# Optimization experiments

Measured on AMD Instinct MI355X. Metric: run time of the kernel, lower is better.

The kernel has to match this reference:

```python
import jax, jax.numpy as jnp
import numpy as np

B, S, D, H = 2, 48, 256, 8
DH = D // H  # depth per head = 32
N = S * S    # flattened pair sequence length = 2304


def setup_inputs() -> dict:
    key = jax.random.key(0)
    ks = jax.random.split(key, 9)
    std = 1.0 / np.sqrt(D)
    x = jax.random.normal(ks[0], (B, S, S, D), dtype=jnp.float32)
    Wq = jax.random.normal(ks[1], (D, D), dtype=jnp.float32) * std
    Wk = jax.random.normal(ks[2], (D, D), dtype=jnp.float32) * std
    Wv = jax.random.normal(ks[3], (D, D), dtype=jnp.float32) * std
    Wo = jax.random.normal(ks[4], (D, D), dtype=jnp.float32) * std
    bq = jnp.zeros((D,), jnp.float32)
    bk = jnp.zeros((D,), jnp.float32)
    bv = jnp.zeros((D,), jnp.float32)
    bo = jnp.zeros((D,), jnp.float32)
    return {"pair_representation": x, "Wq": Wq, "bq": bq, "Wk": Wk, "bk": bk,
            "Wv": Wv, "bv": bv, "Wo": Wo, "bo": bo}


def reference(pair_representation, Wq, bq, Wk, bk, Wv, bv, Wo, bo):
    x = pair_representation.reshape(B, N, D)  # flatten (S,S) -> N

    def heads(t):  # (B,N,D) -> (B,H,N,DH)
        return t.reshape(B, N, H, DH).transpose(0, 2, 1, 3)

    q = heads(x @ Wq + bq)
    k = heads(x @ Wk + bk)
    v = heads(x @ Wv + bv)

    scale = 1.0 / jnp.sqrt(jnp.asarray(DH, jnp.float32))
    logits = jnp.einsum('bhnd,bhmd->bhnm', q, k) * scale  # (B,H,N,N)
    attn = jax.nn.softmax(logits, axis=-1)
    ctx = jnp.einsum('bhnm,bhmd->bhnd', attn, v)
    ctx = ctx.transpose(0, 2, 1, 3).reshape(B, N, D)
    return ctx @ Wo + bo  # (B, N, D)
```

## Files before the change

### kernel.cpp

```cpp
#include <hip/hip_runtime.h>
#include <math.h>

#define B 2
#define S 48
#define D 256
#define H 8
#define DH 32
#define N (S*S)
#define BN (B*N)
#define BH (B*H)
#define KS 4
#define KPZ (N/KS)

typedef _Float16 half8 __attribute__((ext_vector_type(8)));
typedef _Float16 half4_t __attribute__((ext_vector_type(4)));
typedef unsigned short ushort8_t __attribute__((ext_vector_type(8)));
typedef float floatx4 __attribute__((ext_vector_type(4)));

__global__ __launch_bounds__(256) void convert_kernel(
    const float* __restrict__ x,
    const float* __restrict__ Wq, const float* __restrict__ Wk,
    const float* __restrict__ Wv, const float* __restrict__ Wo,
    _Float16* __restrict__ xh, _Float16* __restrict__ xl,
    _Float16* __restrict__ wqh, _Float16* __restrict__ wql,
    _Float16* __restrict__ wkh, _Float16* __restrict__ wkl,
    _Float16* __restrict__ wvh, _Float16* __restrict__ wvl,
    _Float16* __restrict__ woh, _Float16* __restrict__ wol)
{
    const int t = threadIdx.x;
    const int z = blockIdx.y;
    if (z == 0) {
        #pragma unroll
        for (int i = 0; i < 4; i++) {
            int idx = blockIdx.x * 4096 + i * 1024 + t * 4;
            float4 v = *(const float4*)(x + idx);
            float vs[4] = {v.x, v.y, v.z, v.w};
            half4_t hs, ls;
            #pragma unroll
            for (int j = 0; j < 4; j++) {
                _Float16 h = (_Float16)vs[j];
                hs[j] = h;
                ls[j] = (_Float16)(vs[j] - (float)h);
            }
            *(half4_t*)(xh + idx) = hs;
            *(half4_t*)(xl + idx) = ls;
        }
        return;
    }
    if (blockIdx.x >= 16) return;
    const float* W = (z == 1) ? Wq : (z == 2) ? Wk : (z == 3) ? Wv : Wo;
    _Float16* oh   = (z == 1) ? wqh : (z == 2) ? wkh : (z == 3) ? wvh : woh;
    _Float16* ol   = (z == 1) ? wql : (z == 2) ? wkl : (z == 3) ? wvl : wol;
    #pragma unroll
    for (int i = 0; i < 4; i++) {
        int idx = blockIdx.x * 4096 + i * 1024 + t * 4;
        int k = idx >> 8, c = idx & 255;
        float4 v = *(const float4*)(W + idx);
        float vs[4] = {v.x, v.y, v.z, v.w};
        #pragma unroll
        for (int j = 0; j < 4; j++) {
            _Float16 h = (_Float16)vs[j];
            oh[(size_t)(c + j) * D + k] = h;
            ol[(size_t)(c + j) * D + k] = (_Float16)(vs[j] - (float)h);
        }
    }
}

__device__ __forceinline__ void gemm_core(
    const _Float16* __restrict__ Ah, const _Float16* __restrict__ Al,
    const _Float16* __restrict__ Bth, const _Float16* __restrict__ Btl,
    int rowbase, int colbase,
    _Float16* AhS, _Float16* AlS, _Float16* BhS, _Float16* BlS,
    floatx4 acc[4])
{
    const int t = threadIdx.x;
    const int wv = t >> 6, lane = t & 63, l15 = lane & 15, quad = lane >> 4;
    for (int kb = 0; kb < D; kb += 64) {
        __syncthreads();
        #pragma unroll
        for (int i = 0; i < 2; i++) {
            int idx = i * 2048 + t * 8;
            int r = idx >> 6, c = idx & 63;
            *(ushort8_t*)(AhS + r * 72 + c) = *(const ushort8_t*)(Ah + (size_t)(rowbase + r) * D + kb + c);
            *(ushort8_t*)(AlS + r * 72 + c) = *(const ushort8_t*)(Al + (size_t)(rowbase + r) * D + kb + c);
            *(ushort8_t*)(BhS + r * 72 + c) = *(const ushort8_t*)(Bth + (size_t)(colbase + r) * D + kb + c);
            *(ushort8_t*)(BlS + r * 72 + c) = *(const ushort8_t*)(Btl + (size_t)(colbase + r) * D + kb + c);
        }
        __syncthreads();
        #pragma unroll
        for (int ksx = 0; ksx < 2; ksx++) {
            half8 ah = *(const half8*)(AhS + (wv * 16 + l15) * 72 + ksx * 32 + quad * 8);
            half8 al = *(const half8*)(AlS + (wv * 16 + l15) * 72 + ksx * 32 + quad * 8);
            #pragma unroll
            for (int cg = 0; cg < 4; cg++) {
                half8 bh8 = *(const half8*)(BhS + (cg * 16 + l15) * 72 + ksx * 32 + quad * 8);
                half8 bl8 = *(const half8*)(BlS + (cg * 16 + l15) * 72 + ksx * 32 + quad * 8);
                acc[cg] = __builtin_amdgcn_mfma_f32_16x16x32_f16(ah, bh8, acc[cg], 0, 0, 0);
                acc[cg] = __builtin_amdgcn_mfma_f32_16x16x32_f16(al, bh8, acc[cg], 0, 0, 0);
                acc[cg] = __builtin_amdgcn_mfma_f32_16x16x32_f16(ah, bl8, acc[cg], 0, 0, 0);
            }
        }
    }
}

__global__ __launch_bounds__(256) void proj_gemm(
    const _Float16* __restrict__ xh, const _Float16* __restrict__ xl,
    const _Float16* __restrict__ wqh, const _Float16* __restrict__ wql,
    const _Float16* __restrict__ wkh, const _Float16* __restrict__ wkl,
    const _Float16* __restrict__ wvh, const _Float16* __restrict__ wvl,
    const float* __restrict__ bq, const float* __restrict__ bk,
    const float* __restrict__ bv,
    _Float16* __restrict__ qh_o, _Float16* __restrict__ ql_o,
    _Float16* __restrict__ kh_o, _Float16* __restrict__ kl_o,
    _Float16* __restrict__ vh_o)
{
    __shared__ __align__(16) _Float16 AhS[64 * 72];
    __shared__ __align__(16) _Float16 AlS[64 * 72];
    __shared__ __align__(16) _Float16 BhS[64 * 72];
    __shared__ __align__(16) _Float16 BlS[64 * 72];

    const int z = blockIdx.z;
    const _Float16* bth = (z == 0) ? wqh : (z == 1) ? wkh : wvh;
    const _Float16* btl = (z == 0) ? wql : (z == 1) ? wkl : wvl;
    const float* bias   = (z == 0) ? bq : (z == 1) ? bk : bv;
    _Float16* oh        = (z == 0) ? qh_o : (z == 1) ? kh_o : vh_o;
    _Float16* ol        = (z == 0) ? ql_o : kl_o;
    const float scale   = (z == 0) ? rsqrtf((float)DH) : 1.0f;

    const int rowbase = blockIdx.x * 64;
    const int colbase = blockIdx.y * 64;
    floatx4 acc[4] = {{0,0,0,0},{0,0,0,0},{0,0,0,0},{0,0,0,0}};

    gemm_core(xh, xl, bth, btl, rowbase, colbase, AhS, AlS, BhS, BlS, acc);

    const int t = threadIdx.x;
    const int wv = t >> 6, lane = t & 63, l15 = lane & 15, quad = lane >> 4;
    const int b = (rowbase >= N) ? 1 : 0;
    #pragma unroll
    for (int cg = 0; cg < 4; cg++) {
        int col = colbase + cg * 16 + l15;
        int hh = col >> 5, dh = col & 31;
        float bs = bias[col];
        #pragma unroll
        for (int r = 0; r < 4; r++) {
            int n = rowbase + wv * 16 + quad * 4 + r - b * N;
            float v = (acc[cg][r] + bs) * scale;
            size_t ob = ((size_t)(b * H + hh) * N + n) * DH + dh;
            _Float16 hi = (_Float16)v;
            oh[ob] = hi;
            if (z < 2) ol[ob] = (_Float16)(v - (float)hi);
        }
    }
}

__global__ __launch_bounds__(256) void attn_kernel(
    const _Float16* __restrict__ qh, const _Float16* __restrict__ ql,
    const _Float16* __restrict__ kh, const _Float16* __restrict__ kl,
    const _Float16* __restrict__ vh,
    float* __restrict__ ctx_part, float* __restrict__ lpart)
{
    __shared__ __align__(16) _Float16 Kh[64 * 40];
    __shared__ __align__(16) _Float16 Kl[64 * 40];
    __shared__ __align__(16) _Float16 Vt[32 * 72];
    __shared__ __align__(16) _Float16 Ps[4 * 16 * 72];

    const int t = threadIdx.x;
    const int wv = t >> 6, lane = t & 63, l15 = lane & 15, quad = lane >> 4;
    const int bh = blockIdx.y;
    const int kz = blockIdx.z;
    const int qbase = blockIdx.x * 64 + wv * 16;
    _Float16* ps = Ps + wv * 16 * 72;

    const size_t qoff = ((size_t)bh * N + qbase + l15) * DH + quad * 8;
    const half8 a_qh = *(const half8*)(qh + qoff);
    const half8 a_ql = *(const half8*)(ql + qoff);

    floatx4 acc0 = {0,0,0,0}, acc1 = {0,0,0,0};
    float lrow[4] = {0.f, 0.f, 0.f, 0.f};

    const _Float16* kh_g = kh + (size_t)bh * N * DH;
    const _Float16* kl_g = kl + (size_t)bh * N * DH;
    const _Float16* vh_g = vh + (size_t)bh * N * DH;

    const int skey = t >> 2;
    const int sd0  = (t & 3) * 8;
    const int srot = 2 * (t & 3);

    for (int it = 0; it < KPZ / 64; it++) {
        const int key0 = kz * KPZ + it * 64;
        __syncthreads();
        {
            const size_t g = (size_t)key0 * DH + t * 8;
            ushort8_t kv = *(const ushort8_t*)(kh_g + g);
            ushort8_t lv = *(const ushort8_t*)(kl_g + g);
            ushort8_t vv = *(const ushort8_t*)(vh_g + g);
            *(ushort8_t*)(Kh + skey * 40 + sd0) = kv;
            *(ushort8_t*)(Kl + skey * 40 + sd0) = lv;
            unsigned short* vt = (unsigned short*)Vt;
            #pragma unroll
            for (int j = 0; j < 8; j++) {
                int jj = (j + srot) & 7;
                vt[(sd0 + jj) * 72 + skey] = vv[jj];
            }
        }
        __syncthreads();

        floatx4 s[4];
        #pragma unroll
        for (int g = 0; g < 4; g++) {
            half8 bh8 = *(const half8*)(Kh + (g * 16 + l15) * 40 + quad * 8);
            half8 bl8 = *(const half8*)(Kl + (g * 16 + l15) * 40 + quad * 8);
            floatx4 sg = {0,0,0,0};
            sg = __builtin_amdgcn_mfma_f32_16x16x32_f16(a_qh, bh8, sg, 0, 0, 0);
            sg = __builtin_amdgcn_mfma_f32_16x16x32_f16(a_ql, bh8, sg, 0, 0, 0);
            sg = __builtin_amdgcn_mfma_f32_16x16x32_f16(a_qh, bl8, sg, 0, 0, 0);
            s[g] = sg;
        }
        #pragma unroll
        for (int g = 0; g < 4; g++) {
            #pragma unroll
            for (int r = 0; r < 4; r++) {
                float p = __expf(s[g][r]);
                lrow[r] += p;
                ps[(quad * 4 + r) * 72 + g * 16 + l15] = (_Float16)p;
            }
        }
        asm volatile("s_waitcnt lgkmcnt(0)" ::: "memory");

        half8 ap0 = *(const half8*)(ps + l15 * 72 + quad * 8);
        half8 ap1 = *(const half8*)(ps + l15 * 72 + 32 + quad * 8);
        half8 v00 = *(const half8*)(Vt + l15 * 72 + quad * 8);
        half8 v01 = *(const half8*)(Vt + l15 * 72 + 32 + quad * 8);
        half8 v10 = *(const half8*)(Vt + (16 + l15) * 72 + quad * 8);
        half8 v11 = *(const half8*)(Vt + (16 + l15) * 72 + 32 + quad * 8);
        acc0 = __builtin_amdgcn_mfma_f32_16x16x32_f16(ap0, v00, acc0, 0, 0, 0);
        acc0 = __builtin_amdgcn_mfma_f32_16x16x32_f16(ap1, v01, acc0, 0, 0, 0);
        acc1 = __builtin_amdgcn_mfma_f32_16x16x32_f16(ap0, v10, acc1, 0, 0, 0);
        acc1 = __builtin_amdgcn_mfma_f32_16x16x32_f16(ap1, v11, acc1, 0, 0, 0);
    }

    const int b = bh / H, hh = bh % H;
    float* cp = ctx_part + (size_t)kz * BN * D;
    float* lp = lpart + (size_t)kz * BH * N;
    #pragma unroll
    for (int r = 0; r < 4; r++) {
        float ls = lrow[r];
        ls += __shfl_xor(ls, 1); ls += __shfl_xor(ls, 2);
        ls += __shfl_xor(ls, 4); ls += __shfl_xor(ls, 8);
        int qg = qbase + quad * 4 + r;
        float* crow = cp + ((size_t)b * N + qg) * D + hh * DH;
        crow[l15]      = acc0[r];
        crow[16 + l15] = acc1[r];
        if (l15 == 0) lp[bh * N + qg] = ls;
    }
}

__global__ __launch_bounds__(256) void merge_kernel(
    const float* __restrict__ ctx_part, const float* __restrict__ lpart,
    _Float16* __restrict__ ch, _Float16* __restrict__ cl)
{
    const int i = (blockIdx.x * 256 + threadIdx.x) * 4;
    const int row = i >> 8, c = i & 255;
    const int b = (row >= N) ? 1 : 0;
    const int n = row - b * N;
    const int bhn = (b * H + (c >> 5)) * N + n;
    float ls = lpart[bhn] + lpart[BH * N + bhn]
             + lpart[2 * BH * N + bhn] + lpart[3 * BH * N + bhn];
    float inv = 1.0f / ls;
    const float* p = ctx_part + (size_t)row * D + c;
    const size_t st = (size_t)BN * D;
    float4 v0 = *(const float4*)(p);
    float4 v1 = *(const float4*)(p + st);
    float4 v2 = *(const float4*)(p + 2 * st);
    float4 v3 = *(const float4*)(p + 3 * st);
    float vs[4] = {(v0.x + v1.x + v2.x + v3.x) * inv,
                   (v0.y + v1.y + v2.y + v3.y) * inv,
                   (v0.z + v1.z + v2.z + v3.z) * inv,
                   (v0.w + v1.w + v2.w + v3.w) * inv};
    half4_t hs, lo;
    #pragma unroll
    for (int j = 0; j < 4; j++) {
        _Float16 h = (_Float16)vs[j];
        hs[j] = h;
        lo[j] = (_Float16)(vs[j] - (float)h);
    }
    *(half4_t*)(ch + i) = hs;
    *(half4_t*)(cl + i) = lo;
}

__global__ __launch_bounds__(256) void outproj_gemm(
    const _Float16* __restrict__ ch, const _Float16* __restrict__ cl,
    const _Float16* __restrict__ woh, const _Float16* __restrict__ wol,
    const float* __restrict__ bo, float* __restrict__ out)
{
    __shared__ __align__(16) _Float16 AhS[64 * 72];
    __shared__ __align__(16) _Float16 AlS[64 * 72];
    __shared__ __align__(16) _Float16 BhS[64 * 72];
    __shared__ __align__(16) _Float16 BlS[64 * 72];

    const int rowbase = blockIdx.x * 64;
    const int colbase = blockIdx.y * 64;
    floatx4 acc[4] = {{0,0,0,0},{0,0,0,0},{0,0,0,0},{0,0,0,0}};

    gemm_core(ch, cl, woh, wol, rowbase, colbase, AhS, AlS, BhS, BlS, acc);

    const int t = threadIdx.x;
    const int wv = t >> 6, lane = t & 63, l15 = lane & 15, quad = lane >> 4;
    #pragma unroll
    for (int cg = 0; cg < 4; cg++) {
        int col = colbase + cg * 16 + l15;
        float bs = bo[col];
        #pragma unroll
        for (int r = 0; r < 4; r++) {
            int row = rowbase + wv * 16 + quad * 4 + r;
            out[(size_t)row * D + col] = acc[cg][r] + bs;
        }
    }
}

extern "C" void kernel_launch(void* const* d_in, const int* in_sizes, int n_in,
                              void* d_out, int out_size, void* d_ws, size_t ws_size,
                              hipStream_t stream)
{
    const float* x  = (const float*)d_in[0];
    const float* Wq = (const float*)d_in[1];
    const float* bq = (const float*)d_in[2];
    const float* Wk = (const float*)d_in[3];
    const float* bk = (const float*)d_in[4];
    const float* Wv = (const float*)d_in[5];
    const float* bv = (const float*)d_in[6];
    const float* Wo = (const float*)d_in[7];
    const float* bo = (const float*)d_in[8];
    float* out = (float*)d_out;

    const size_t NE = (size_t)BN * D;
    const size_t WE = (size_t)D * D;

    float* ctx_part = (float*)d_ws;
    float* lpart    = ctx_part + (size_t)KS * NE;
    _Float16* xh = (_Float16*)(lpart + (size_t)KS * BH * N);
    _Float16* xl = xh + NE;
    _Float16* qh = xl + NE;
    _Float16* ql = qh + NE;
    _Float16* kh = ql + NE;
    _Float16* kl = kh + NE;
    _Float16* vh = kl + NE;
    _Float16* ch = vh + NE;
    _Float16* cl = ch + NE;
    _Float16* wqh = cl + NE;
    _Float16* wql = wqh + WE;
    _Float16* wkh = wql + WE;
    _Float16* wkl = wkh + WE;
    _Float16* wvh = wkl + WE;
    _Float16* wvl = wvh + WE;
    _Float16* woh = wvl + WE;
    _Float16* wol = woh + WE;

    convert_kernel<<<dim3(288, 5), 256, 0, stream>>>(
        x, Wq, Wk, Wv, Wo, xh, xl, wqh, wql, wkh, wkl, wvh, wvl, woh, wol);

    proj_gemm<<<dim3(BN / 64, D / 64, 3), 256, 0, stream>>>(
        xh, xl, wqh, wql, wkh, wkl, wvh, wvl, bq, bk, bv,
        qh, ql, kh, kl, vh);

    attn_kernel<<<dim3(N / 64, BH, KS), 256, 0, stream>>>(
        qh, ql, kh, kl, vh, ctx_part, lpart);

    merge_kernel<<<dim3(BN * D / 1024), 256, 0, stream>>>(
        ctx_part, lpart, ch, cl);

    outproj_gemm<<<dim3(BN / 64, D / 64), 256, 0, stream>>>(
        ch, cl, woh, wol, bo, out);
}
```

Measured before the change: 148.8 us.

## Fuse input split and merge into GEMMs, restructure attention to register-resident P

The fp32-to-fp16 hi/lo split of x moves into the projection GEMM's tile load. The split-K merge and normalisation move into the output-projection GEMM's A-tile load, which removes the separate convert and merge kernels and their intermediate buffers. The attention kernel is restructured to compute S^T with 16x16x16 MFMAs so the exp'd probabilities stay in registers as the B operand for PV. This drops the LDS round-trip for P, and exp2 is used with log2e folded into the Q scale. Weight conversion now transposes through shared memory for coalesced writes, but the fused loads redo split and merge work for each of the four column blocks.

```diff
diff --git a/kernel.cpp b/kernel.cpp
--- a/kernel.cpp
+++ b/kernel.cpp
@@ -11,17 +11,26 @@
 #define BH (B*H)
 #define KS 4
 #define KPZ (N/KS)
+#define NE ((size_t)BN*D)
+#define BHN (BH*N)
 
 typedef _Float16 half8 __attribute__((ext_vector_type(8)));
 typedef _Float16 half4_t __attribute__((ext_vector_type(4)));
 typedef unsigned short ushort8_t __attribute__((ext_vector_type(8)));
 typedef float floatx4 __attribute__((ext_vector_type(4)));
 
-__global__ __launch_bounds__(256) void convert_kernel(
-    const float* __restrict__ x,
+__device__ __forceinline__ void split8(const float* v, half8* hi, half8* lo) {
+    #pragma unroll
+    for (int j = 0; j < 8; j++) {
+        _Float16 h = (_Float16)v[j];
+        (*hi)[j] = h;
+        (*lo)[j] = (_Float16)(v[j] - (float)h);
+    }
+}
+
+__global__ __launch_bounds__(256) void convert_w(
     const float* __restrict__ Wq, const float* __restrict__ Wk,
     const float* __restrict__ Wv, const float* __restrict__ Wo,
-    _Float16* __restrict__ xh, _Float16* __restrict__ xl,
     _Float16* __restrict__ wqh, _Float16* __restrict__ wql,
     _Float16* __restrict__ wkh, _Float16* __restrict__ wkl,
     _Float16* __restrict__ wvh, _Float16* __restrict__ wvl,
@@ -29,82 +38,37 @@
 {
     const int t = threadIdx.x;
     const int z = blockIdx.y;
-    if (z == 0) {
-        #pragma unroll
-        for (int i = 0; i < 4; i++) {
-            int idx = blockIdx.x * 4096 + i * 1024 + t * 4;
-            float4 v = *(const float4*)(x + idx);
-            float vs[4] = {v.x, v.y, v.z, v.w};
-            half4_t hs, ls;
-            #pragma unroll
-            for (int j = 0; j < 4; j++) {
-                _Float16 h = (_Float16)vs[j];
-                hs[j] = h;
-                ls[j] = (_Float16)(vs[j] - (float)h);
-            }
-            *(half4_t*)(xh + idx) = hs;
-            *(half4_t*)(xl + idx) = ls;
-        }
-        return;
-    }
-    if (blockIdx.x >= 16) return;
-    const float* W = (z == 1) ? Wq : (z == 2) ? Wk : (z == 3) ? Wv : Wo;
-    _Float16* oh   = (z == 1) ? wqh : (z == 2) ? wkh : (z == 3) ? wvh : woh;
-    _Float16* ol   = (z == 1) ? wql : (z == 2) ? wkl : (z == 3) ? wvl : wol;
+    const int tr = blockIdx.x >> 2, tc = blockIdx.x & 3;
+    const float* W = (z == 0) ? Wq : (z == 1) ? Wk : (z == 2) ? Wv : Wo;
+    _Float16* oh   = (z == 0) ? wqh : (z == 1) ? wkh : (z == 2) ? wvh : woh;
+    _Float16* ol   = (z == 0) ? wql : (z == 1) ? wkl : (z == 2) ? wvl : wol;
+
+    __shared__ float Ws[64 * 68];
     #pragma unroll
     for (int i = 0; i < 4; i++) {
-        int idx = blockIdx.x * 4096 + i * 1024 + t * 4;
-        int k = idx >> 8, c = idx & 255;
-        float4 v = *(const float4*)(W + idx);
-        float vs[4] = {v.x, v.y, v.z, v.w};
-        #pragma unroll
-        for (int j = 0; j < 4; j++) {
-            _Float16 h = (_Float16)vs[j];
-            oh[(size_t)(c + j) * D + k] = h;
-            ol[(size_t)(c + j) * D + k] = (_Float16)(vs[j] - (float)h);
-        }
-    }
-}
-
-__device__ __forceinline__ void gemm_core(
-    const _Float16* __restrict__ Ah, const _Float16* __restrict__ Al,
-    const _Float16* __restrict__ Bth, const _Float16* __restrict__ Btl,
-    int rowbase, int colbase,
-    _Float16* AhS, _Float16* AlS, _Float16* BhS, _Float16* BlS,
-    floatx4 acc[4])
-{
-    const int t = threadIdx.x;
-    const int wv = t >> 6, lane = t & 63, l15 = lane & 15, quad = lane >> 4;
-    for (int kb = 0; kb < D; kb += 64) {
-        __syncthreads();
-        #pragma unroll
-        for (int i = 0; i < 2; i++) {
-            int idx = i * 2048 + t * 8;
-            int r = idx >> 6, c = idx & 63;
-            *(ushort8_t*)(AhS + r * 72 + c) = *(const ushort8_t*)(Ah + (size_t)(rowbase + r) * D + kb + c);
-            *(ushort8_t*)(AlS + r * 72 + c) = *(const ushort8_t*)(Al + (size_t)(rowbase + r) * D + kb + c);
-            *(ushort8_t*)(BhS + r * 72 + c) = *(const ushort8_t*)(Bth + (size_t)(colbase + r) * D + kb + c);
-            *(ushort8_t*)(BlS + r * 72 + c) = *(const ushort8_t*)(Btl + (size_t)(colbase + r) * D + kb + c);
-        }
-        __syncthreads();
-        #pragma unroll
-        for (int ksx = 0; ksx < 2; ksx++) {
-            half8 ah = *(const half8*)(AhS + (wv * 16 + l15) * 72 + ksx * 32 + quad * 8);
-            half8 al = *(const half8*)(AlS + (wv * 16 + l15) * 72 + ksx * 32 + quad * 8);
-            #pragma unroll
-            for (int cg = 0; cg < 4; cg++) {
-                half8 bh8 = *(const half8*)(BhS + (cg * 16 + l15) * 72 + ksx * 32 + quad * 8);
-                half8 bl8 = *(const half8*)(BlS + (cg * 16 + l15) * 72 + ksx * 32 + quad * 8);
-                acc[cg] = __builtin_amdgcn_mfma_f32_16x16x32_f16(ah, bh8, acc[cg], 0, 0, 0);
-                acc[cg] = __builtin_amdgcn_mfma_f32_16x16x32_f16(al, bh8, acc[cg], 0, 0, 0);
-                acc[cg] = __builtin_amdgcn_mfma_f32_16x16x32_f16(ah, bl8, acc[cg], 0, 0, 0);
-            }
-        }
+        int idx = i * 1024 + t * 4;
+        int r = idx >> 6, c = idx & 63;
+        *(float4*)(&Ws[r * 68 + c]) =
+            *(const float4*)(W + (size_t)(tr * 64 + r) * D + tc * 64 + c);
+    }
+    __syncthreads();
+    #pragma unroll
+    for (int it = 0; it < 2; it++) {
+        int idx = it * 256 + t;
+        int cc = idx & 63, k0 = (idx >> 6) * 8;
+        float v[8];
+        #pragma unroll
+        for (int j = 0; j < 8; j++) v[j] = Ws[(k0 + j) * 68 + cc];
+        half8 hi, lo;
+        split8(v, &hi, &lo);
+        size_t ob = (size_t)(tc * 64 + cc) * D + tr * 64 + k0;
+        *(half8*)(oh + ob) = hi;
+        *(half8*)(ol + ob) = lo;
     }
 }
 
 __global__ __launch_bounds__(256) void proj_gemm(
-    const _Float16* __restrict__ xh, const _Float16* __restrict__ xl,
+    const float* __restrict__ x,
     const _Float16* __restrict__ wqh, const _Float16* __restrict__ wql,
     const _Float16* __restrict__ wkh, const _Float16* __restrict__ wkl,
     const _Float16* __restrict__ wvh, const _Float16* __restrict__ wvl,
@@ -125,17 +89,50 @@
     const float* bias   = (z == 0) ? bq : (z == 1) ? bk : bv;
     _Float16* oh        = (z == 0) ? qh_o : (z == 1) ? kh_o : vh_o;
     _Float16* ol        = (z == 0) ? ql_o : kl_o;
-    const float scale   = (z == 0) ? rsqrtf((float)DH) : 1.0f;
-
+    const float scale   = (z == 0) ? rsqrtf((float)DH) * 1.44269504f : 1.0f;
+
+    const int t = threadIdx.x;
+    const int wv2 = t >> 6, lane = t & 63, l15 = lane & 15, quad = lane >> 4;
     const int rowbase = blockIdx.x * 64;
     const int colbase = blockIdx.y * 64;
     floatx4 acc[4] = {{0,0,0,0},{0,0,0,0},{0,0,0,0},{0,0,0,0}};
 
-    gemm_core(xh, xl, bth, btl, rowbase, colbase, AhS, AlS, BhS, BlS, acc);
-
-    const int t = threadIdx.x;
-    const int wv = t >> 6, lane = t & 63, l15 = lane & 15, quad = lane >> 4;
-    const int b = (rowbase >= N) ? 1 : 0;
+    for (int kb = 0; kb < D; kb += 64) {
+        __syncthreads();
+        #pragma unroll
+        for (int i = 0; i < 2; i++) {
+            int idx = i * 2048 + t * 8;
+            int r = idx >> 6, c = idx & 63;
+            const float* xp = x + (size_t)(rowbase + r) * D + kb + c;
+            float4 x0 = *(const float4*)xp;
+            float4 x1 = *(const float4*)(xp + 4);
+            float v[8] = {x0.x, x0.y, x0.z, x0.w, x1.x, x1.y, x1.z, x1.w};
+            half8 hi, lo;
+            split8(v, &hi, &lo);
+            *(half8*)(AhS + r * 72 + c) = hi;
+            *(half8*)(AlS + r * 72 + c) = lo;
+            *(ushort8_t*)(BhS + r * 72 + c) =
+                *(const ushort8_t*)(bth + (size_t)(colbase + r) * D + kb + c);
+            *(ushort8_t*)(BlS + r * 72 + c) =
+                *(const ushort8_t*)(btl + (size_t)(colbase + r) * D + kb + c);
+        }
+        __syncthreads();
+        #pragma unroll
+        for (int ksx = 0; ksx < 2; ksx++) {
+            half8 ah = *(const half8*)(AhS + (wv2 * 16 + l15) * 72 + ksx * 32 + quad * 8);
+            half8 al = *(const half8*)(AlS + (wv2 * 16 + l15) * 72 + ksx * 32 + quad * 8);
+            #pragma unroll
+            for (int cg = 0; cg < 4; cg++) {
+                half8 bh8 = *(const half8*)(BhS + (cg * 16 + l15) * 72 + ksx * 32 + quad * 8);
+                half8 bl8 = *(const half8*)(BlS + (cg * 16 + l15) * 72 + ksx * 32 + quad * 8);
+                acc[cg] = __builtin_amdgcn_mfma_f32_16x16x32_f16(ah, bh8, acc[cg], 0, 0, 0);
+                acc[cg] = __builtin_amdgcn_mfma_f32_16x16x32_f16(al, bh8, acc[cg], 0, 0, 0);
+                acc[cg] = __builtin_amdgcn_mfma_f32_16x16x32_f16(ah, bl8, acc[cg], 0, 0, 0);
+            }
+        }
+    }
+
+    const int bb = (rowbase >= N) ? 1 : 0;
     #pragma unroll
     for (int cg = 0; cg < 4; cg++) {
         int col = colbase + cg * 16 + l15;
@@ -143,9 +140,9 @@
         float bs = bias[col];
         #pragma unroll
         for (int r = 0; r < 4; r++) {
-            int n = rowbase + wv * 16 + quad * 4 + r - b * N;
+            int n = rowbase + wv2 * 16 + quad * 4 + r - bb * N;
             float v = (acc[cg][r] + bs) * scale;
-            size_t ob = ((size_t)(b * H + hh) * N + n) * DH + dh;
+            size_t ob = ((size_t)(bb * H + hh) * N + n) * DH + dh;
             _Float16 hi = (_Float16)v;
             oh[ob] = hi;
             if (z < 2) ol[ob] = (_Float16)(v - (float)hi);
@@ -162,21 +159,24 @@
     __shared__ __align__(16) _Float16 Kh[64 * 40];
     __shared__ __align__(16) _Float16 Kl[64 * 40];
     __shared__ __align__(16) _Float16 Vt[32 * 72];
-    __shared__ __align__(16) _Float16 Ps[4 * 16 * 72];
 
     const int t = threadIdx.x;
-    const int wv = t >> 6, lane = t & 63, l15 = lane & 15, quad = lane >> 4;
-    const int bh = blockIdx.y;
-    const int kz = blockIdx.z;
-    const int qbase = blockIdx.x * 64 + wv * 16;
-    _Float16* ps = Ps + wv * 16 * 72;
-
-    const size_t qoff = ((size_t)bh * N + qbase + l15) * DH + quad * 8;
-    const half8 a_qh = *(const half8*)(qh + qoff);
-    const half8 a_ql = *(const half8*)(ql + qoff);
-
-    floatx4 acc0 = {0,0,0,0}, acc1 = {0,0,0,0};
-    float lrow[4] = {0.f, 0.f, 0.f, 0.f};
+    const int wv2 = t >> 6, lane = t & 63, l15 = lane & 15, quad = lane >> 4;
+    const int bh = blockIdx.y, kz = blockIdx.z;
+    const int qbase = blockIdx.x * 128 + wv2 * 32;
+
+    half4_t bqh[2][2], bql[2][2];
+    #pragma unroll
+    for (int qg = 0; qg < 2; qg++) {
+        const size_t qoff = ((size_t)bh * N + qbase + qg * 16 + l15) * DH + quad * 4;
+        bqh[qg][0] = *(const half4_t*)(qh + qoff);
+        bqh[qg][1] = *(const half4_t*)(qh + qoff + 16);
+        bql[qg][0] = *(const half4_t*)(ql + qoff);
+        bql[qg][1] = *(const half4_t*)(ql + qoff + 16);
+    }
+
+    floatx4 acc[2][2] = {{{0,0,0,0},{0,0,0,0}},{{0,0,0,0},{0,0,0,0}}};
+    float lsum[2] = {0.f, 0.f};
 
     const _Float16* kh_g = kh + (size_t)bh * N * DH;
     const _Float16* kl_g = kl + (size_t)bh * N * DH;
@@ -205,91 +205,58 @@
         }
         __syncthreads();
 
-        floatx4 s[4];
-        #pragma unroll
-        for (int g = 0; g < 4; g++) {
-            half8 bh8 = *(const half8*)(Kh + (g * 16 + l15) * 40 + quad * 8);
-            half8 bl8 = *(const half8*)(Kl + (g * 16 + l15) * 40 + quad * 8);
-            floatx4 sg = {0,0,0,0};
-            sg = __builtin_amdgcn_mfma_f32_16x16x32_f16(a_qh, bh8, sg, 0, 0, 0);
-            sg = __builtin_amdgcn_mfma_f32_16x16x32_f16(a_ql, bh8, sg, 0, 0, 0);
-            sg = __builtin_amdgcn_mfma_f32_16x16x32_f16(a_qh, bl8, sg, 0, 0, 0);
-            s[g] = sg;
-        }
-        #pragma unroll
-        for (int g = 0; g < 4; g++) {
-            #pragma unroll
-            for (int r = 0; r < 4; r++) {
-                float p = __expf(s[g][r]);
-                lrow[r] += p;
-                ps[(quad * 4 + r) * 72 + g * 16 + l15] = (_Float16)p;
+        #pragma unroll
+        for (int kg = 0; kg < 4; kg++) {
+            const _Float16* kr = Kh + (kg * 16 + l15) * 40 + quad * 4;
+            const _Float16* lr = Kl + (kg * 16 + l15) * 40 + quad * 4;
+            half4_t ah0 = *(const half4_t*)(kr);
+            half4_t ah1 = *(const half4_t*)(kr + 16);
+            half4_t al0 = *(const half4_t*)(lr);
+            half4_t al1 = *(const half4_t*)(lr + 16);
+            half4_t va0 = *(const half4_t*)(Vt + l15 * 72 + kg * 16 + quad * 4);
+            half4_t va1 = *(const half4_t*)(Vt + (16 + l15) * 72 + kg * 16 + quad * 4);
+            #pragma unroll
+            for (int qg = 0; qg < 2; qg++) {
+                floatx4 s = {0, 0, 0, 0};
+                s = __builtin_amdgcn_mfma_f32_16x16x16f16(ah0, bqh[qg][0], s, 0, 0, 0);
+                s = __builtin_amdgcn_mfma_f32_16x16x16f16(al0, bqh[qg][0], s, 0, 0, 0);
+                s = __builtin_amdgcn_mfma_f32_16x16x16f16(ah0, bql[qg][0], s, 0, 0, 0);
+                s = __builtin_amdgcn_mfma_f32_16x16x16f16(ah1, bqh[qg][1], s, 0, 0, 0);
+                s = __builtin_amdgcn_mfma_f32_16x16x16f16(al1, bqh[qg][1], s, 0, 0, 0);
+                s = __builtin_amdgcn_mfma_f32_16x16x16f16(ah1, bql[qg][1], s, 0, 0, 0);
+                float p0 = exp2f(s[0]), p1 = exp2f(s[1]);
+                float p2 = exp2f(s[2]), p3 = exp2f(s[3]);
+                lsum[qg] += (p0 + p1) + (p2 + p3);
+                half4_t pf;
+                pf[0] = (_Float16)p0; pf[1] = (_Float16)p1;
+                pf[2] = (_Float16)p2; pf[3] = (_Float16)p3;
+                acc[qg][0] = __builtin_amdgcn_mfma_f32_16x16x16f16(va0, pf, acc[qg][0], 0, 0, 0);
+                acc[qg][1] = __builtin_amdgcn_mfma_f32_16x16x16f16(va1, pf, acc[qg][1], 0, 0, 0);
             }
         }
-        asm volatile("s_waitcnt lgkmcnt(0)" ::: "memory");
-
-        half8 ap0 = *(const half8*)(ps + l15 * 72 + quad * 8);
-        half8 ap1 = *(const half8*)(ps + l15 * 72 + 32 + quad * 8);
-        half8 v00 = *(const half8*)(Vt + l15 * 72 + quad * 8);
-        half8 v01 = *(const half8*)(Vt + l15 * 72 + 32 + quad * 8);
-        half8 v10 = *(const half8*)(Vt + (16 + l15) * 72 + quad * 8);
-        half8 v11 = *(const half8*)(Vt + (16 + l15) * 72 + 32 + quad * 8);
-        acc0 = __builtin_amdgcn_mfma_f32_16x16x32_f16(ap0, v00, acc0, 0, 0, 0);
-        acc0 = __builtin_amdgcn_mfma_f32_16x16x32_f16(ap1, v01, acc0, 0, 0, 0);
-        acc1 = __builtin_amdgcn_mfma_f32_16x16x32_f16(ap0, v10, acc1, 0, 0, 0);
-        acc1 = __builtin_amdgcn_mfma_f32_16x16x32_f16(ap1, v11, acc1, 0, 0, 0);
-    }
-
-    const int b = bh / H, hh = bh % H;
-    float* cp = ctx_part + (size_t)kz * BN * D;
-    float* lp = lpart + (size_t)kz * BH * N;
-    #pragma unroll
-    for (int r = 0; r < 4; r++) {
-        float ls = lrow[r];
-        ls += __shfl_xor(ls, 1); ls += __shfl_xor(ls, 2);
-        ls += __shfl_xor(ls, 4); ls += __shfl_xor(ls, 8);
-        int qg = qbase + quad * 4 + r;
-        float* crow = cp + ((size_t)b * N + qg) * D + hh * DH;
-        crow[l15]      = acc0[r];
-        crow[16 + l15] = acc1[r];
-        if (l15 == 0) lp[bh * N + qg] = ls;
-    }
-}
-
-__global__ __launch_bounds__(256) void merge_kernel(
+    }
+
+    const int bb = bh / H, hh = bh % H;
+    float* cp = ctx_part + (size_t)kz * NE;
+    float* lp = lpart + (size_t)kz * BHN;
+    #pragma unroll
+    for (int qg = 0; qg < 2; qg++) {
+        float ls = lsum[qg];
+        ls += __shfl_xor(ls, 16);
+        ls += __shfl_xor(ls, 32);
+        int q = qbase + qg * 16 + l15;
+        if (quad == 0) lp[bh * N + q] = ls;
+        float* crow = cp + ((size_t)bb * N + q) * D + hh * DH;
+        #pragma unroll
+        for (int dg = 0; dg < 2; dg++)
+            #pragma unroll
+            for (int r = 0; r < 4; r++)
+                crow[dg * 16 + quad * 4 + r] = acc[qg][dg][r];
+    }
+}
+
+__global__ __launch_bounds__(256) void outproj_gemm(
     const float* __restrict__ ctx_part, const float* __restrict__ lpart,
-    _Float16* __restrict__ ch, _Float16* __restrict__ cl)
-{
-    const int i = (blockIdx.x * 256 + threadIdx.x) * 4;
-    const int row = i >> 8, c = i & 255;
-    const int b = (row >= N) ? 1 : 0;
-    const int n = row - b * N;
-    const int bhn = (b * H + (c >> 5)) * N + n;
-    float ls = lpart[bhn] + lpart[BH * N + bhn]
-             + lpart[2 * BH * N + bhn] + lpart[3 * BH * N + bhn];
-    float inv = 1.0f / ls;
-    const float* p = ctx_part + (size_t)row * D + c;
-    const size_t st = (size_t)BN * D;
-    float4 v0 = *(const float4*)(p);
-    float4 v1 = *(const float4*)(p + st);
-    float4 v2 = *(const float4*)(p + 2 * st);
-    float4 v3 = *(const float4*)(p + 3 * st);
-    float vs[4] = {(v0.x + v1.x + v2.x + v3.x) * inv,
-                   (v0.y + v1.y + v2.y + v3.y) * inv,
-                   (v0.z + v1.z + v2.z + v3.z) * inv,
-                   (v0.w + v1.w + v2.w + v3.w) * inv};
-    half4_t hs, lo;
-    #pragma unroll
-    for (int j = 0; j < 4; j++) {
-        _Float16 h = (_Float16)vs[j];
-        hs[j] = h;
-        lo[j] = (_Float16)(vs[j] - (float)h);
-    }
-    *(half4_t*)(ch + i) = hs;
-    *(half4_t*)(cl + i) = lo;
-}
-
-__global__ __launch_bounds__(256) void outproj_gemm(
-    const _Float16* __restrict__ ch, const _Float16* __restrict__ cl,
     const _Float16* __restrict__ woh, const _Float16* __restrict__ wol,
     const float* __restrict__ bo, float* __restrict__ out)
 {
@@ -298,21 +265,71 @@
     __shared__ __align__(16) _Float16 BhS[64 * 72];
     __shared__ __align__(16) _Float16 BlS[64 * 72];
 
+    const int t = threadIdx.x;
+    const int wv2 = t >> 6, lane = t & 63, l15 = lane & 15, quad = lane >> 4;
     const int rowbase = blockIdx.x * 64;
     const int colbase = blockIdx.y * 64;
     floatx4 acc[4] = {{0,0,0,0},{0,0,0,0},{0,0,0,0},{0,0,0,0}};
 
-    gemm_core(ch, cl, woh, wol, rowbase, colbase, AhS, AlS, BhS, BlS, acc);
-
-    const int t = threadIdx.x;
-    const int wv = t >> 6, lane = t & 63, l15 = lane & 15, quad = lane >> 4;
+    for (int kb = 0; kb < D; kb += 64) {
+        __syncthreads();
+        #pragma unroll
+        for (int i = 0; i < 2; i++) {
+            int idx = i * 2048 + t * 8;
+            int r = idx >> 6, c = idx & 63;
+            int row = rowbase + r;
+            int kcol = kb + c;
+            int bb = (row >= N) ? 1 : 0;
+            int n = row - bb * N;
+            int bhn = (bb * H + (kcol >> 5)) * N + n;
+            float ls = lpart[bhn] + lpart[BHN + bhn]
+                     + lpart[2 * BHN + bhn] + lpart[3 * BHN + bhn];
+            float inv = 1.0f / ls;
+            const float* pp = ctx_part + (size_t)row * D + kcol;
+            float4 a0 = *(const float4*)(pp),          a1 = *(const float4*)(pp + 4);
+            float4 b0 = *(const float4*)(pp + NE),     b1 = *(const float4*)(pp + NE + 4);
+            float4 c0 = *(const float4*)(pp + 2 * NE), c1 = *(const float4*)(pp + 2 * NE + 4);
+            float4 d0 = *(const float4*)(pp + 3 * NE), d1 = *(const float4*)(pp + 3 * NE + 4);
+            float v[8] = {(a0.x + b0.x + c0.x + d0.x) * inv,
+                          (a0.y + b0.y + c0.y + d0.y) * inv,
+                          (a0.z + b0.z + c0.z + d0.z) * inv,
+                          (a0.w + b0.w + c0.w + d0.w) * inv,
+                          (a1.x + b1.x + c1.x + d1.x) * inv,
+                          (a1.y + b1.y + c1.y + d1.y) * inv,
+                          (a1.z + b1.z + c1.z + d1.z) * inv,
+                          (a1.w + b1.w + c1.w + d1.w) * inv};
+            half8 hi, lo;
+            split8(v, &hi, &lo);
+            *(half8*)(AhS + r * 72 + c) = hi;
+            *(half8*)(AlS + r * 72 + c) = lo;
+            *(ushort8_t*)(BhS + r * 72 + c) =
+                *(const ushort8_t*)(woh + (size_t)(colbase + r) * D + kb + c);
+            *(ushort8_t*)(BlS + r * 72 + c) =
+                *(const ushort8_t*)(wol + (size_t)(colbase + r) * D + kb + c);
+        }
+        __syncthreads();
+        #pragma unroll
+        for (int ksx = 0; ksx < 2; ksx++) {
+            half8 ah = *(const half8*)(AhS + (wv2 * 16 + l15) * 72 + ksx * 32 + quad * 8);
+            half8 al = *(const half8*)(AlS + (wv2 * 16 + l15) * 72 + ksx * 32 + quad * 8);
+            #pragma unroll
+            for (int cg = 0; cg < 4; cg++) {
+                half8 bh8 = *(const half8*)(BhS + (cg * 16 + l15) * 72 + ksx * 32 + quad * 8);
+                half8 bl8 = *(const half8*)(BlS + (cg * 16 + l15) * 72 + ksx * 32 + quad * 8);
+                acc[cg] = __builtin_amdgcn_mfma_f32_16x16x32_f16(ah, bh8, acc[cg], 0, 0, 0);
+                acc[cg] = __builtin_amdgcn_mfma_f32_16x16x32_f16(al, bh8, acc[cg], 0, 0, 0);
+                acc[cg] = __builtin_amdgcn_mfma_f32_16x16x32_f16(ah, bl8, acc[cg], 0, 0, 0);
+            }
+        }
+    }
+
     #pragma unroll
     for (int cg = 0; cg < 4; cg++) {
         int col = colbase + cg * 16 + l15;
         float bs = bo[col];
         #pragma unroll
         for (int r = 0; r < 4; r++) {
-            int row = rowbase + wv * 16 + quad * 4 + r;
+            int row = rowbase + wv2 * 16 + quad * 4 + r;
             out[(size_t)row * D + col] = acc[cg][r] + bs;
         }
     }
@@ -333,21 +350,16 @@
     const float* bo = (const float*)d_in[8];
     float* out = (float*)d_out;
 
-    const size_t NE = (size_t)BN * D;
     const size_t WE = (size_t)D * D;
 
     float* ctx_part = (float*)d_ws;
     float* lpart    = ctx_part + (size_t)KS * NE;
-    _Float16* xh = (_Float16*)(lpart + (size_t)KS * BH * N);
-    _Float16* xl = xh + NE;
-    _Float16* qh = xl + NE;
-    _Float16* ql = qh + NE;
-    _Float16* kh = ql + NE;
-    _Float16* kl = kh + NE;
-    _Float16* vh = kl + NE;
-    _Float16* ch = vh + NE;
-    _Float16* cl = ch + NE;
-    _Float16* wqh = cl + NE;
+    _Float16* qh  = (_Float16*)(lpart + (size_t)KS * BHN);
+    _Float16* ql  = qh + NE;
+    _Float16* kh  = ql + NE;
+    _Float16* kl  = kh + NE;
+    _Float16* vh  = kl + NE;
+    _Float16* wqh = vh + NE;
     _Float16* wql = wqh + WE;
     _Float16* wkh = wql + WE;
     _Float16* wkl = wkh + WE;
@@ -356,19 +368,16 @@
     _Float16* woh = wvl + WE;
     _Float16* wol = woh + WE;
 
-    convert_kernel<<<dim3(288, 5), 256, 0, stream>>>(
-        x, Wq, Wk, Wv, Wo, xh, xl, wqh, wql, wkh, wkl, wvh, wvl, woh, wol);
+    convert_w<<<dim3(16, 4), 256, 0, stream>>>(
+        Wq, Wk, Wv, Wo, wqh, wql, wkh, wkl, wvh, wvl, woh, wol);
 
     proj_gemm<<<dim3(BN / 64, D / 64, 3), 256, 0, stream>>>(
-        xh, xl, wqh, wql, wkh, wkl, wvh, wvl, bq, bk, bv,
+        x, wqh, wql, wkh, wkl, wvh, wvl, bq, bk, bv,
         qh, ql, kh, kl, vh);
 
-    attn_kernel<<<dim3(N / 64, BH, KS), 256, 0, stream>>>(
+    attn_kernel<<<dim3(N / 128, BH, KS), 256, 0, stream>>>(
         qh, ql, kh, kl, vh, ctx_part, lpart);
 
-    merge_kernel<<<dim3(BN * D / 1024), 256, 0, stream>>>(
-        ctx_part, lpart, ch, cl);
-
     outproj_gemm<<<dim3(BN / 64, D / 64), 256, 0, stream>>>(
-        ch, cl, woh, wol, bo, out);
-}
+        ctx_part, lpart, woh, wol, bo, out);
+}
```

Result: slower. 156.4 us (+5.1%).
